# Kernel tuning notes

Hardware: AMD Instinct MI355X
Metric: run time of the kernel (lower is better)

## Reference

```python
import jax, jax.numpy as jnp
import numpy as np
from itertools import chain, combinations

OBS_DIM = 4096
LAT = 64
NG = 4
GS = OBS_DIM // NG  # 1024 features per group (round-robin i % NG == g)
B = 8192


def _powerset_mask(n):
    subsets = list(chain.from_iterable(combinations(range(n), r) for r in range(1, n + 1)))
    m = np.zeros((len(subsets), n), np.float32)
    for i, s in enumerate(subsets):
        m[i, list(s)] = 1.0
    return jnp.asarray(m)


SUBSET_MASK = _powerset_mask(NG)  # [S, G], S = 2^G - 1 = 15
GROUP_IDX = jnp.asarray(np.stack([np.arange(g, OBS_DIM, NG) for g in range(NG)]), dtype=jnp.int32)  # [G, GS]


def setup_inputs() -> dict:
    key = jax.random.key(0)
    ks = jax.random.split(key, 11)
    s = 0.05
    H = 2 * LAT  # encoder hidden / output width
    return {
        "X": jax.random.normal(ks[0], (B, OBS_DIM), jnp.float32),
        "eps": jax.random.normal(ks[1], (B, LAT), jnp.float32),
        "subset_idx": jax.random.randint(ks[2], (B,), 0, SUBSET_MASK.shape[0], dtype=jnp.int32),
        "enc_w1": jax.random.normal(ks[3], (NG, GS, H), jnp.float32) * s,
        "enc_b1": jnp.zeros((NG, H), jnp.float32),
        "enc_w2": jax.random.normal(ks[4], (NG, H, H), jnp.float32) * s,
        "enc_b2": jnp.zeros((NG, H), jnp.float32),
        "dec_w1": jax.random.normal(ks[5], (NG, LAT, LAT), jnp.float32) * s,
        "dec_b1": jnp.zeros((NG, LAT), jnp.float32),
        "dec_w2": jax.random.normal(ks[6], (NG, LAT, GS), jnp.float32) * s,
        "dec_b2": jnp.zeros((NG, GS), jnp.float32),
    }


def reference(X, eps, subset_idx, enc_w1, enc_b1, enc_w2, enc_b2, dec_w1, dec_b1, dec_w2, dec_b2):
    # ---- encode: per-group gather + tiny MLP (depth=2) ----
    Xg = X[:, GROUP_IDX]  # [B, G, GS] gather of group columns
    h = jax.nn.relu(jnp.einsum('bgi,gih->bgh', Xg, enc_w1) + enc_b1[None])  # [B, G, 2L]
    ml = jnp.einsum('bgh,gho->bgo', h, enc_w2) + enc_b2[None]               # [B, G, 2L]
    means, logvars = jnp.split(ml, 2, axis=-1)  # each [B, G, L]
    means = jnp.transpose(means, (0, 2, 1))     # [B, L, G] (tf stacks groups on axis=2)
    logvars = jnp.transpose(logvars, (0, 2, 1))

    # ---- mopoe: PoE over every non-empty subset of groups ----
    taus = jnp.exp(-logvars)                                   # [B, L, G]
    tau = jnp.einsum('blg,sg->bls', taus, SUBSET_MASK) + 1.0   # [B, L, S] (normalize_outp=True adds 1)
    m_means = jnp.einsum('blg,sg->bls', taus * means, SUBSET_MASK) / tau
    m_logvars = -jnp.log(tau)                                  # log(1/tau)

    # ---- reparameterize: pick one random subset per batch row ----
    sel = subset_idx[:, None, None].astype(jnp.int32)          # [B, 1, 1]
    smean = jnp.take_along_axis(m_means, sel, axis=-1)[..., 0]    # [B, L]
    slogv = jnp.take_along_axis(m_logvars, sel, axis=-1)[..., 0]  # [B, L]
    z = smean + eps * jnp.exp(0.5 * slogv)                     # [B, L]

    # ---- decode: per-group tiny MLP, scatter back to obs_dim ----
    hd = jax.nn.relu(jnp.einsum('bl,glm->bgm', z, dec_w1) + dec_b1[None])  # [B, G, L]
    outg = jnp.einsum('bgm,gmo->bgo', hd, dec_w2) + dec_b2[None]            # [B, G, GS]
    recon = jnp.zeros((X.shape[0], OBS_DIM), X.dtype).at[:, GROUP_IDX.reshape(-1)].set(
        outg.reshape(X.shape[0], -1))
    return recon
```

## Files before the change

### kernel.cpp

```cpp
#include <hip/hip_runtime.h>
#include <hip/hip_bf16.h>
#include <math.h>

#define B_TOT 8192
#define OBS   4096
#define NG    4
#define GSZ   1024
#define LATD  64
#define HDIM  128

typedef __attribute__((ext_vector_type(8))) short   short8_t;
typedef __attribute__((ext_vector_type(8))) unsigned short ushort8_t;
typedef __attribute__((ext_vector_type(4))) float   float4_t;

__constant__ int kMask[15] = {1,2,4,8, 3,5,9,6,10,12, 7,11,13,14, 15};

static __device__ __forceinline__ unsigned short f2b(float x) {
  __hip_bfloat16 b = __float2bfloat16(x);
  return *reinterpret_cast<unsigned short*>(&b);
}
static __device__ __forceinline__ unsigned int pack2(float lo, float hi) {
  return (unsigned int)f2b(lo) | ((unsigned int)f2b(hi) << 16);
}

#define N1 524288
#define N2 65536
#define N4 262144
__global__ __launch_bounds__(256) void k_prep(const float* __restrict__ w1,
                                              const float* __restrict__ w2,
                                              const float* __restrict__ w4,
                                              unsigned short* __restrict__ W1t,
                                              unsigned short* __restrict__ W2t,
                                              unsigned short* __restrict__ W4t) {
  const int i = blockIdx.x * 256 + threadIdx.x;
  if (i < N1) {
    const int g = i >> 17, rem = i & 131071;
    const int h = rem >> 10, k = rem & 1023;
    W1t[i] = f2b(w1[g * 131072 + k * 128 + h]);
  } else if (i < N1 + N2) {
    const int idx = i - N1;
    const int g = idx >> 14, rem = idx & 16383;
    const int o = rem >> 7, k = rem & 127;
    W2t[idx] = f2b(w2[g * 16384 + k * 128 + o]);
  } else {
    const int idx = i - N1 - N2;
    const int g = idx >> 16, rem = idx & 65535;
    const int o = rem >> 6, k = rem & 63;
    W4t[idx] = f2b(w4[g * 65536 + k * 1024 + o]);
  }
}

__global__ __launch_bounds__(512, 2) void k_enc1(const float* __restrict__ X,
                                                 const unsigned short* __restrict__ W1t,
                                                 const float* __restrict__ B1,
                                                 unsigned short* __restrict__ Hbf) {
  __shared__ unsigned short lA[4][4][32][40];

  const int tid = threadIdx.x;
  const int w   = tid >> 6;
  const int l   = tid & 63;
  const int g   = w >> 1;
  const int hh  = (w & 1) * 64;
  const int r0b = blockIdx.x * 32;
  const int l15 = l & 15;
  const int oct = l >> 4;

  const int sr  = tid >> 4;
  const int skk = tid & 15;

  const float* xrow = X + (size_t)(r0b + sr) * OBS;

  float4 q[4][2];
#pragma unroll
  for (int sub = 0; sub < 4; ++sub) {
    const float* p = xrow + sub * 128 + skk * 8;
    q[sub][0] = *(const float4*)(p);
    q[sub][1] = *(const float4*)(p + 4);
  }

  float4_t acc[2][4];
#pragma unroll
  for (int i = 0; i < 2; ++i)
#pragma unroll
    for (int j = 0; j < 4; ++j) acc[i][j] = (float4_t){0.f, 0.f, 0.f, 0.f};

  for (int c = 0; c < 8; ++c) {
#pragma unroll
    for (int sub = 0; sub < 4; ++sub) {
      const float a0[4] = {q[sub][0].x, q[sub][0].y, q[sub][0].z, q[sub][0].w};
      const float a1[4] = {q[sub][1].x, q[sub][1].y, q[sub][1].z, q[sub][1].w};
#pragma unroll
      for (int gg = 0; gg < 4; ++gg)
        *(unsigned int*)(&lA[sub][gg][sr][skk * 2]) = pack2(a0[gg], a1[gg]);
    }
    __syncthreads();

    if (c < 7) {
      const float* base = xrow + (c + 1) * 512;
#pragma unroll
      for (int sub = 0; sub < 4; ++sub) {
        const float* p = base + sub * 128 + skk * 8;
        q[sub][0] = *(const float4*)(p);
        q[sub][1] = *(const float4*)(p + 4);
      }
    }

#pragma unroll
    for (int sub = 0; sub < 4; ++sub) {
      short8_t af[2], bf[4];
#pragma unroll
      for (int mi = 0; mi < 2; ++mi)
        af[mi] = *(const short8_t*)((const char*)&lA[sub][g][0][0] +
                                    (mi * 16 + l15) * 80 + oct * 16);
#pragma unroll
      for (int ni = 0; ni < 4; ++ni)
        bf[ni] = *(const short8_t*)(W1t +
                  (size_t)(g * 128 + hh + ni * 16 + l15) * 1024 +
                  c * 128 + sub * 32 + oct * 8);
#pragma unroll
      for (int mi = 0; mi < 2; ++mi)
#pragma unroll
        for (int ni = 0; ni < 4; ++ni)
          acc[mi][ni] = __builtin_amdgcn_mfma_f32_16x16x32_bf16(af[mi], bf[ni], acc[mi][ni], 0, 0, 0);
    }
    __syncthreads();
  }

#pragma unroll
  for (int ni = 0; ni < 4; ++ni) {
    const int col = g * 128 + hh + ni * 16 + l15;
    const float b = B1[col];
#pragma unroll
    for (int mi = 0; mi < 2; ++mi) {
      const int rbase = r0b + mi * 16 + oct * 4;
#pragma unroll
      for (int j = 0; j < 4; ++j)
        Hbf[(size_t)(rbase + j) * 512 + col] = f2b(fmaxf(acc[mi][ni][j] + b, 0.0f));
    }
  }
}

struct Enc2Lds {
  union {
    unsigned short A[16][1288];
    float mls[32][516];
  };
};
__global__ __launch_bounds__(512, 2) void k_enc2_samp(const unsigned short* __restrict__ Hbf,
                                                      const unsigned short* __restrict__ W2t,
                                                      const float* __restrict__ B2,
                                                      const float* __restrict__ eps,
                                                      const int*   __restrict__ subset_idx,
                                                      float* __restrict__ Z) {
  __shared__ Enc2Lds u;
  const int tid = threadIdx.x;
  const int w   = tid >> 6;
  const int l   = tid & 63;
  const int g   = w >> 1;
  const int hh  = (w & 1) * 64;
  const int rb  = blockIdx.x * 32;
  const int l15 = l & 15;
  const int oct = l >> 4;

#pragma unroll
  for (int i = 0; i < 4; ++i) {
    const int q   = tid + i * 512;
    const int row = q >> 6;
    const int co  = (q & 63) * 8;
    const int gg  = co >> 7;
    const int cg  = co & 127;
    const int ks  = cg >> 5;
    const int off = cg & 31;
    const ushort8_t v = *(const ushort8_t*)(Hbf + (size_t)(rb + row) * 512 + co);
    *(ushort8_t*)(&u.A[ks * 4 + gg][row * 40 + off]) = v;
  }
  __syncthreads();

  float4_t acc[2][4];
#pragma unroll
  for (int i = 0; i < 2; ++i)
#pragma unroll
    for (int j = 0; j < 4; ++j) acc[i][j] = (float4_t){0.f, 0.f, 0.f, 0.f};

#pragma unroll
  for (int ks = 0; ks < 4; ++ks) {
    short8_t af[2], bf[4];
#pragma unroll
    for (int mi = 0; mi < 2; ++mi)
      af[mi] = *(const short8_t*)(&u.A[ks * 4 + g][(mi * 16 + l15) * 40 + oct * 8]);
#pragma unroll
    for (int ni = 0; ni < 4; ++ni)
      bf[ni] = *(const short8_t*)(W2t +
                (size_t)(g * 128 + hh + ni * 16 + l15) * 128 + ks * 32 + oct * 8);
#pragma unroll
    for (int mi = 0; mi < 2; ++mi)
#pragma unroll
      for (int ni = 0; ni < 4; ++ni)
        acc[mi][ni] = __builtin_amdgcn_mfma_f32_16x16x32_bf16(af[mi], bf[ni], acc[mi][ni], 0, 0, 0);
  }
  __syncthreads();

#pragma unroll
  for (int ni = 0; ni < 4; ++ni) {
    const int col = g * 128 + hh + ni * 16 + l15;
    const float b = B2[col];
#pragma unroll
    for (int mi = 0; mi < 2; ++mi)
#pragma unroll
      for (int j = 0; j < 4; ++j)
        u.mls[mi * 16 + oct * 4 + j][col] = acc[mi][ni][j] + b;
  }
  __syncthreads();

#pragma unroll
  for (int q = 0; q < 4; ++q) {
    const int idx = q * 512 + tid;
    const int r   = idx >> 6;
    const int ll  = idx & 63;
    const int m   = kMask[subset_idx[rb + r]];
    float tau = 1.0f, num = 0.0f;
#pragma unroll
    for (int gg = 0; gg < 4; ++gg) {
      if (m & (1 << gg)) {
        const float lv = u.mls[r][gg * 128 + 64 + ll];
        const float mu = u.mls[r][gg * 128 + ll];
        const float t  = expf(-lv);
        tau += t;
        num = fmaf(t, mu, num);
      }
    }
    Z[(size_t)(rb + r) * LATD + ll] =
        num / tau + eps[(size_t)(rb + r) * LATD + ll] * rsqrtf(tau);
  }
}

__global__ __launch_bounds__(256) void k_dec1(const float* __restrict__ Z,
                                              const float* __restrict__ W,
                                              const float* __restrict__ Bb,
                                              unsigned short* __restrict__ Hd) {
  const int tid  = threadIdx.x;
  const int wid  = tid >> 6;
  const int lane = tid & 63;
  const int r0   = blockIdx.x * 16 + wid * 4;
  const int c0   = lane * 4;
  const int g    = c0 >> 6;
  const int m0   = c0 & 63;

  const float* Wp = W + (size_t)g * LATD * LATD + m0;
  const float* Ap = Z + (size_t)r0 * LATD;

  float acc[4][4];
#pragma unroll
  for (int i = 0; i < 4; ++i)
#pragma unroll
    for (int j = 0; j < 4; ++j) acc[i][j] = 0.0f;

#pragma unroll 4
  for (int k = 0; k < LATD; ++k) {
    const float4 wv = *(const float4*)(Wp + (size_t)k * LATD);
    float a[4];
#pragma unroll
    for (int i = 0; i < 4; ++i) a[i] = Ap[(size_t)i * LATD + k];
#pragma unroll
    for (int i = 0; i < 4; ++i) {
      acc[i][0] = fmaf(a[i], wv.x, acc[i][0]);
      acc[i][1] = fmaf(a[i], wv.y, acc[i][1]);
      acc[i][2] = fmaf(a[i], wv.z, acc[i][2]);
      acc[i][3] = fmaf(a[i], wv.w, acc[i][3]);
    }
  }

  const float4 ba = *(const float4*)(Bb + c0);
#pragma unroll
  for (int i = 0; i < 4; ++i) {
    ushort4 o;
    o.x = f2b(fmaxf(acc[i][0] + ba.x, 0.0f));
    o.y = f2b(fmaxf(acc[i][1] + ba.y, 0.0f));
    o.z = f2b(fmaxf(acc[i][2] + ba.z, 0.0f));
    o.w = f2b(fmaxf(acc[i][3] + ba.w, 0.0f));
    *(ushort4*)(Hd + (size_t)(r0 + i) * 256 + c0) = o;
  }
}

__global__ __launch_bounds__(512) void k_dec2(const unsigned short* __restrict__ Hd,
                                              const unsigned short* __restrict__ W4t,
                                              const float* __restrict__ Bb,
                                              float* __restrict__ Out) {
  __shared__ float obuf[32][264];

  const int tid = threadIdx.x;
  const int w   = tid >> 6;
  const int l   = tid & 63;
  const int g   = w >> 1;
  const int ohh = (w & 1) * 32;
  const int r0  = blockIdx.x * 32;
  const int ob  = blockIdx.y * 64;
  const int l15 = l & 15;
  const int oct = l >> 4;

  float4_t acc[2][2];
#pragma unroll
  for (int i = 0; i < 2; ++i)
#pragma unroll
    for (int j = 0; j < 2; ++j) acc[i][j] = (float4_t){0.f, 0.f, 0.f, 0.f};

#pragma unroll
  for (int ks = 0; ks < 2; ++ks) {
    short8_t af[2], bf[2];
#pragma unroll
    for (int mi = 0; mi < 2; ++mi)
      af[mi] = *(const short8_t*)(Hd + (size_t)(r0 + mi * 16 + l15) * 256 +
                                  g * 64 + ks * 32 + oct * 8);
#pragma unroll
    for (int ni = 0; ni < 2; ++ni)
      bf[ni] = *(const short8_t*)(W4t + (size_t)(g * 1024 + ob + ohh + ni * 16 + l15) * 64 +
                                  ks * 32 + oct * 8);
#pragma unroll
    for (int mi = 0; mi < 2; ++mi)
#pragma unroll
      for (int ni = 0; ni < 2; ++ni)
        acc[mi][ni] = __builtin_amdgcn_mfma_f32_16x16x32_bf16(af[mi], bf[ni], acc[mi][ni], 0, 0, 0);
  }

#pragma unroll
  for (int ni = 0; ni < 2; ++ni) {
    const int lo = ohh + ni * 16 + l15;
    const float b = Bb[g * 1024 + ob + lo];
#pragma unroll
    for (int mi = 0; mi < 2; ++mi) {
      const int rloc = mi * 16 + oct * 4;
#pragma unroll
      for (int j = 0; j < 4; ++j)
        obuf[rloc + j][4 * lo + g] = acc[mi][ni][j] + b;
    }
  }
  __syncthreads();

#pragma unroll
  for (int i = 0; i < 4; ++i) {
    const int q = tid + i * 512;
    const int row = q >> 6, c4 = q & 63;
    const float4 v = *(const float4*)&obuf[row][c4 * 4];
    *(float4*)(Out + (size_t)(r0 + row) * OBS + 4 * ob + c4 * 4) = v;
  }
}

extern "C" void kernel_launch(void* const* d_in, const int* in_sizes, int n_in,
                              void* d_out, int out_size, void* d_ws, size_t ws_size,
                              hipStream_t stream) {
  const float* X          = (const float*)d_in[0];
  const float* eps        = (const float*)d_in[1];
  const int*   subset_idx = (const int*)  d_in[2];
  const float* enc_w1     = (const float*)d_in[3];
  const float* enc_b1     = (const float*)d_in[4];
  const float* enc_w2     = (const float*)d_in[5];
  const float* enc_b2     = (const float*)d_in[6];
  const float* dec_w1     = (const float*)d_in[7];
  const float* dec_b1     = (const float*)d_in[8];
  const float* dec_w2     = (const float*)d_in[9];
  const float* dec_b2     = (const float*)d_in[10];
  float* out = (float*)d_out;

  char* wsb = (char*)d_ws;
  unsigned short* Hbf = (unsigned short*)wsb;
  float*          z   = (float*)(wsb + (8u  << 20));
  unsigned short* Hd  = (unsigned short*)(wsb + (10u << 20));
  unsigned short* W1t = (unsigned short*)(wsb + (14u << 20));
  unsigned short* W2t = (unsigned short*)(wsb + (15u << 20));
  unsigned short* W4t = (unsigned short*)(wsb + (15u << 20) + (512u << 10));

  k_prep<<<3328, 256, 0, stream>>>(enc_w1, enc_w2, dec_w2, W1t, W2t, W4t);
  k_enc1<<<256, 512, 0, stream>>>(X, W1t, enc_b1, Hbf);
  k_enc2_samp<<<256, 512, 0, stream>>>(Hbf, W2t, enc_b2, eps, subset_idx, z);
  k_dec1<<<512, 256, 0, stream>>>(z, dec_w1, dec_b1, Hd);
  k_dec2<<<dim3(256, 16), 512, 0, stream>>>(Hd, W4t, dec_b2, out);
}
```

Measured before the change: 127.3 us.

## Fuse encoder layers, sampling and first decoder layer; pre-convert X to bf16

Adds a separate pass that converts X to bf16 in a group-deinterleaved layout written to workspace. The two encoder GEMMs, the PoE sampling and the first decoder layer are merged into one kernel. The first decoder layer now runs on MFMA using a prepared bf16 weight instead of scalar fp32 FMAs. This removes the Hbf and z round-trips and two launches. In exchange it writes and re-reads a 64MB bf16 copy of X, and the first-layer GEMM loses its LDS staging and register prefetch, so it now reads strided rows straight from global memory.

```diff
diff --git a/kernel.cpp b/kernel.cpp
--- a/kernel.cpp
+++ b/kernel.cpp
@@ -25,12 +25,15 @@
 
 #define N1 524288
 #define N2 65536
+#define N3 16384
 #define N4 262144
 __global__ __launch_bounds__(256) void k_prep(const float* __restrict__ w1,
                                               const float* __restrict__ w2,
+                                              const float* __restrict__ w3,
                                               const float* __restrict__ w4,
                                               unsigned short* __restrict__ W1t,
                                               unsigned short* __restrict__ W2t,
+                                              unsigned short* __restrict__ W3t,
                                               unsigned short* __restrict__ W4t) {
   const int i = blockIdx.x * 256 + threadIdx.x;
   if (i < N1) {
@@ -42,117 +45,52 @@
     const int g = idx >> 14, rem = idx & 16383;
     const int o = rem >> 7, k = rem & 127;
     W2t[idx] = f2b(w2[g * 16384 + k * 128 + o]);
-  } else {
+  } else if (i < N1 + N2 + N3) {
     const int idx = i - N1 - N2;
+    const int g = idx >> 12, rem = idx & 4095;
+    const int m = rem >> 6, k = rem & 63;
+    W3t[idx] = f2b(w3[g * 4096 + k * 64 + m]);
+  } else if (i < N1 + N2 + N3 + N4) {
+    const int idx = i - N1 - N2 - N3;
     const int g = idx >> 16, rem = idx & 65535;
     const int o = rem >> 6, k = rem & 63;
     W4t[idx] = f2b(w4[g * 65536 + k * 1024 + o]);
   }
 }
 
-__global__ __launch_bounds__(512, 2) void k_enc1(const float* __restrict__ X,
-                                                 const unsigned short* __restrict__ W1t,
-                                                 const float* __restrict__ B1,
-                                                 unsigned short* __restrict__ Hbf) {
-  __shared__ unsigned short lA[4][4][32][40];
-
-  const int tid = threadIdx.x;
-  const int w   = tid >> 6;
-  const int l   = tid & 63;
-  const int g   = w >> 1;
-  const int hh  = (w & 1) * 64;
-  const int r0b = blockIdx.x * 32;
-  const int l15 = l & 15;
-  const int oct = l >> 4;
-
-  const int sr  = tid >> 4;
-  const int skk = tid & 15;
-
-  const float* xrow = X + (size_t)(r0b + sr) * OBS;
-
-  float4 q[4][2];
-#pragma unroll
-  for (int sub = 0; sub < 4; ++sub) {
-    const float* p = xrow + sub * 128 + skk * 8;
-    q[sub][0] = *(const float4*)(p);
-    q[sub][1] = *(const float4*)(p + 4);
-  }
-
-  float4_t acc[2][4];
-#pragma unroll
-  for (int i = 0; i < 2; ++i)
-#pragma unroll
-    for (int j = 0; j < 4; ++j) acc[i][j] = (float4_t){0.f, 0.f, 0.f, 0.f};
-
-  for (int c = 0; c < 8; ++c) {
-#pragma unroll
-    for (int sub = 0; sub < 4; ++sub) {
-      const float a0[4] = {q[sub][0].x, q[sub][0].y, q[sub][0].z, q[sub][0].w};
-      const float a1[4] = {q[sub][1].x, q[sub][1].y, q[sub][1].z, q[sub][1].w};
-#pragma unroll
-      for (int gg = 0; gg < 4; ++gg)
-        *(unsigned int*)(&lA[sub][gg][sr][skk * 2]) = pack2(a0[gg], a1[gg]);
-    }
-    __syncthreads();
-
-    if (c < 7) {
-      const float* base = xrow + (c + 1) * 512;
-#pragma unroll
-      for (int sub = 0; sub < 4; ++sub) {
-        const float* p = base + sub * 128 + skk * 8;
-        q[sub][0] = *(const float4*)(p);
-        q[sub][1] = *(const float4*)(p + 4);
-      }
-    }
-
-#pragma unroll
-    for (int sub = 0; sub < 4; ++sub) {
-      short8_t af[2], bf[4];
-#pragma unroll
-      for (int mi = 0; mi < 2; ++mi)
-        af[mi] = *(const short8_t*)((const char*)&lA[sub][g][0][0] +
-                                    (mi * 16 + l15) * 80 + oct * 16);
-#pragma unroll
-      for (int ni = 0; ni < 4; ++ni)
-        bf[ni] = *(const short8_t*)(W1t +
-                  (size_t)(g * 128 + hh + ni * 16 + l15) * 1024 +
-                  c * 128 + sub * 32 + oct * 8);
-#pragma unroll
-      for (int mi = 0; mi < 2; ++mi)
-#pragma unroll
-        for (int ni = 0; ni < 4; ++ni)
-          acc[mi][ni] = __builtin_amdgcn_mfma_f32_16x16x32_bf16(af[mi], bf[ni], acc[mi][ni], 0, 0, 0);
-    }
-    __syncthreads();
-  }
-
-#pragma unroll
-  for (int ni = 0; ni < 4; ++ni) {
-    const int col = g * 128 + hh + ni * 16 + l15;
-    const float b = B1[col];
-#pragma unroll
-    for (int mi = 0; mi < 2; ++mi) {
-      const int rbase = r0b + mi * 16 + oct * 4;
-#pragma unroll
-      for (int j = 0; j < 4; ++j)
-        Hbf[(size_t)(rbase + j) * 512 + col] = f2b(fmaxf(acc[mi][ni][j] + b, 0.0f));
-    }
-  }
-}
-
-struct Enc2Lds {
+__global__ __launch_bounds__(512) void k_prepx(const float* __restrict__ X,
+                                               unsigned short* __restrict__ Xt) {
+  const int b = blockIdx.x;
+  const int t = threadIdx.x;
+  const float* p = X + (size_t)b * OBS + t * 8;
+  const float4 f0 = *(const float4*)(p);
+  const float4 f1 = *(const float4*)(p + 4);
+  const float a0[4] = {f0.x, f0.y, f0.z, f0.w};
+  const float a1[4] = {f1.x, f1.y, f1.z, f1.w};
+  unsigned int* q = (unsigned int*)(Xt + (size_t)b * OBS);
+#pragma unroll
+  for (int g = 0; g < 4; ++g)
+    q[g * 512 + t] = pack2(a0[g], a1[g]);
+}
+
+struct EncLds {
   union {
-    unsigned short A[16][1288];
+    unsigned short hp[16][32][40];
     float mls[32][516];
-  };
+  } u;
+  unsigned short zb[32][72];
 };
-__global__ __launch_bounds__(512, 2) void k_enc2_samp(const unsigned short* __restrict__ Hbf,
-                                                      const unsigned short* __restrict__ W2t,
-                                                      const float* __restrict__ B2,
-                                                      const float* __restrict__ eps,
-                                                      const int*   __restrict__ subset_idx,
-                                                      float* __restrict__ Z) {
-  __shared__ Enc2Lds u;
+__global__ __launch_bounds__(512, 2) void k_enc(const unsigned short* __restrict__ Xt,
+                                                const unsigned short* __restrict__ W1t,
+                                                const unsigned short* __restrict__ W2t,
+                                                const unsigned short* __restrict__ W3t,
+                                                const float* __restrict__ B1,
+                                                const float* __restrict__ B2,
+                                                const float* __restrict__ DB1,
+                                                const float* __restrict__ eps,
+                                                const int*   __restrict__ subset_idx,
+                                                unsigned short* __restrict__ Hd) {
+  __shared__ EncLds s;
   const int tid = threadIdx.x;
   const int w   = tid >> 6;
   const int l   = tid & 63;
@@ -162,41 +100,69 @@
   const int l15 = l & 15;
   const int oct = l >> 4;
 
-#pragma unroll
-  for (int i = 0; i < 4; ++i) {
-    const int q   = tid + i * 512;
-    const int row = q >> 6;
-    const int co  = (q & 63) * 8;
-    const int gg  = co >> 7;
-    const int cg  = co & 127;
-    const int ks  = cg >> 5;
-    const int off = cg & 31;
-    const ushort8_t v = *(const ushort8_t*)(Hbf + (size_t)(rb + row) * 512 + co);
-    *(ushort8_t*)(&u.A[ks * 4 + gg][row * 40 + off]) = v;
-  }
-  __syncthreads();
-
   float4_t acc[2][4];
 #pragma unroll
   for (int i = 0; i < 2; ++i)
 #pragma unroll
     for (int j = 0; j < 4; ++j) acc[i][j] = (float4_t){0.f, 0.f, 0.f, 0.f};
 
-#pragma unroll
-  for (int ks = 0; ks < 4; ++ks) {
-    short8_t af[2], bf[4];
-#pragma unroll
-    for (int mi = 0; mi < 2; ++mi)
-      af[mi] = *(const short8_t*)(&u.A[ks * 4 + g][(mi * 16 + l15) * 40 + oct * 8]);
-#pragma unroll
-    for (int ni = 0; ni < 4; ++ni)
-      bf[ni] = *(const short8_t*)(W2t +
-                (size_t)(g * 128 + hh + ni * 16 + l15) * 128 + ks * 32 + oct * 8);
-#pragma unroll
-    for (int mi = 0; mi < 2; ++mi)
+  {
+    const unsigned short* abase = Xt + (size_t)(rb + l15) * OBS + g * GSZ + oct * 8;
+    const unsigned short* bbase = W1t + (size_t)(g * 128 + hh + l15) * GSZ + oct * 8;
+#pragma unroll 4
+    for (int ks = 0; ks < 32; ++ks) {
+      short8_t af[2], bf[4];
+#pragma unroll
+      for (int mi = 0; mi < 2; ++mi)
+        af[mi] = *(const short8_t*)(abase + (size_t)mi * 16 * OBS + ks * 32);
 #pragma unroll
       for (int ni = 0; ni < 4; ++ni)
-        acc[mi][ni] = __builtin_amdgcn_mfma_f32_16x16x32_bf16(af[mi], bf[ni], acc[mi][ni], 0, 0, 0);
+        bf[ni] = *(const short8_t*)(bbase + (size_t)ni * 16 * GSZ + ks * 32);
+#pragma unroll
+      for (int mi = 0; mi < 2; ++mi)
+#pragma unroll
+        for (int ni = 0; ni < 4; ++ni)
+          acc[mi][ni] = __builtin_amdgcn_mfma_f32_16x16x32_bf16(af[mi], bf[ni], acc[mi][ni], 0, 0, 0);
+    }
+  }
+
+#pragma unroll
+  for (int ni = 0; ni < 4; ++ni) {
+    const int cg    = hh + ni * 16 + l15;
+    const int plane = (cg >> 5) * 4 + g;
+    const int off   = cg & 31;
+    const float b   = B1[g * 128 + cg];
+#pragma unroll
+    for (int mi = 0; mi < 2; ++mi) {
+      const int row = mi * 16 + oct * 4;
+#pragma unroll
+      for (int j = 0; j < 4; ++j)
+        s.u.hp[plane][row + j][off] = f2b(fmaxf(acc[mi][ni][j] + b, 0.0f));
+    }
+  }
+  __syncthreads();
+
+#pragma unroll
+  for (int i = 0; i < 2; ++i)
+#pragma unroll
+    for (int j = 0; j < 4; ++j) acc[i][j] = (float4_t){0.f, 0.f, 0.f, 0.f};
+  {
+    const unsigned short* bbase = W2t + (size_t)(g * 128 + hh + l15) * HDIM + oct * 8;
+#pragma unroll
+    for (int ks = 0; ks < 4; ++ks) {
+      short8_t af[2], bf[4];
+#pragma unroll
+      for (int mi = 0; mi < 2; ++mi)
+        af[mi] = *(const short8_t*)(&s.u.hp[ks * 4 + g][mi * 16 + l15][oct * 8]);
+#pragma unroll
+      for (int ni = 0; ni < 4; ++ni)
+        bf[ni] = *(const short8_t*)(bbase + (size_t)ni * 16 * HDIM + ks * 32);
+#pragma unroll
+      for (int mi = 0; mi < 2; ++mi)
+#pragma unroll
+        for (int ni = 0; ni < 4; ++ni)
+          acc[mi][ni] = __builtin_amdgcn_mfma_f32_16x16x32_bf16(af[mi], bf[ni], acc[mi][ni], 0, 0, 0);
+    }
   }
   __syncthreads();
 
@@ -208,7 +174,7 @@
     for (int mi = 0; mi < 2; ++mi)
 #pragma unroll
       for (int j = 0; j < 4; ++j)
-        u.mls[mi * 16 + oct * 4 + j][col] = acc[mi][ni][j] + b;
+        s.u.mls[mi * 16 + oct * 4 + j][col] = acc[mi][ni][j] + b;
   }
   __syncthreads();
 
@@ -222,63 +188,53 @@
 #pragma unroll
     for (int gg = 0; gg < 4; ++gg) {
       if (m & (1 << gg)) {
-        const float lv = u.mls[r][gg * 128 + 64 + ll];
-        const float mu = u.mls[r][gg * 128 + ll];
+        const float lv = s.u.mls[r][gg * 128 + 64 + ll];
+        const float mu = s.u.mls[r][gg * 128 + ll];
         const float t  = expf(-lv);
         tau += t;
         num = fmaf(t, mu, num);
       }
     }
-    Z[(size_t)(rb + r) * LATD + ll] =
-        num / tau + eps[(size_t)(rb + r) * LATD + ll] * rsqrtf(tau);
-  }
-}
-
-__global__ __launch_bounds__(256) void k_dec1(const float* __restrict__ Z,
-                                              const float* __restrict__ W,
-                                              const float* __restrict__ Bb,
-                                              unsigned short* __restrict__ Hd) {
-  const int tid  = threadIdx.x;
-  const int wid  = tid >> 6;
-  const int lane = tid & 63;
-  const int r0   = blockIdx.x * 16 + wid * 4;
-  const int c0   = lane * 4;
-  const int g    = c0 >> 6;
-  const int m0   = c0 & 63;
-
-  const float* Wp = W + (size_t)g * LATD * LATD + m0;
-  const float* Ap = Z + (size_t)r0 * LATD;
-
-  float acc[4][4];
-#pragma unroll
-  for (int i = 0; i < 4; ++i)
-#pragma unroll
-    for (int j = 0; j < 4; ++j) acc[i][j] = 0.0f;
-
-#pragma unroll 4
-  for (int k = 0; k < LATD; ++k) {
-    const float4 wv = *(const float4*)(Wp + (size_t)k * LATD);
-    float a[4];
-#pragma unroll
-    for (int i = 0; i < 4; ++i) a[i] = Ap[(size_t)i * LATD + k];
-#pragma unroll
-    for (int i = 0; i < 4; ++i) {
-      acc[i][0] = fmaf(a[i], wv.x, acc[i][0]);
-      acc[i][1] = fmaf(a[i], wv.y, acc[i][1]);
-      acc[i][2] = fmaf(a[i], wv.z, acc[i][2]);
-      acc[i][3] = fmaf(a[i], wv.w, acc[i][3]);
-    }
-  }
-
-  const float4 ba = *(const float4*)(Bb + c0);
-#pragma unroll
-  for (int i = 0; i < 4; ++i) {
-    ushort4 o;
-    o.x = f2b(fmaxf(acc[i][0] + ba.x, 0.0f));
-    o.y = f2b(fmaxf(acc[i][1] + ba.y, 0.0f));
-    o.z = f2b(fmaxf(acc[i][2] + ba.z, 0.0f));
-    o.w = f2b(fmaxf(acc[i][3] + ba.w, 0.0f));
-    *(ushort4*)(Hd + (size_t)(r0 + i) * 256 + c0) = o;
+    const float zv = num / tau + eps[(size_t)(rb + r) * LATD + ll] * rsqrtf(tau);
+    s.zb[r][ll] = f2b(zv);
+  }
+  __syncthreads();
+
+  const int mh = (w & 1) * 32;
+  float4_t a3[2][2];
+#pragma unroll
+  for (int i = 0; i < 2; ++i)
+#pragma unroll
+    for (int j = 0; j < 2; ++j) a3[i][j] = (float4_t){0.f, 0.f, 0.f, 0.f};
+  {
+    const unsigned short* bbase = W3t + (size_t)(g * 64 + mh + l15) * LATD + oct * 8;
+#pragma unroll
+    for (int ks = 0; ks < 2; ++ks) {
+      short8_t af[2], bf[2];
+#pragma unroll
+      for (int mi = 0; mi < 2; ++mi)
+        af[mi] = *(const short8_t*)(&s.zb[mi * 16 + l15][ks * 32 + oct * 8]);
+#pragma unroll
+      for (int ni = 0; ni < 2; ++ni)
+        bf[ni] = *(const short8_t*)(bbase + (size_t)ni * 16 * LATD + ks * 32);
+#pragma unroll
+      for (int mi = 0; mi < 2; ++mi)
+#pragma unroll
+        for (int ni = 0; ni < 2; ++ni)
+          a3[mi][ni] = __builtin_amdgcn_mfma_f32_16x16x32_bf16(af[mi], bf[ni], a3[mi][ni], 0, 0, 0);
+    }
+  }
+#pragma unroll
+  for (int ni = 0; ni < 2; ++ni) {
+    const int col = g * 64 + mh + ni * 16 + l15;
+    const float b = DB1[col];
+#pragma unroll
+    for (int mi = 0; mi < 2; ++mi) {
+      const int row = mi * 16 + oct * 4;
+#pragma unroll
+      for (int j = 0; j < 4; ++j)
+        Hd[(size_t)(rb + row + j) * 256 + col] = f2b(fmaxf(a3[mi][ni][j] + b, 0.0f));
+    }
   }
 }
 
@@ -362,16 +318,17 @@
   float* out = (float*)d_out;
 
   char* wsb = (char*)d_ws;
-  unsigned short* Hbf = (unsigned short*)wsb;
-  float*          z   = (float*)(wsb + (8u  << 20));
-  unsigned short* Hd  = (unsigned short*)(wsb + (10u << 20));
-  unsigned short* W1t = (unsigned short*)(wsb + (14u << 20));
-  unsigned short* W2t = (unsigned short*)(wsb + (15u << 20));
-  unsigned short* W4t = (unsigned short*)(wsb + (15u << 20) + (512u << 10));
-
-  k_prep<<<3328, 256, 0, stream>>>(enc_w1, enc_w2, dec_w2, W1t, W2t, W4t);
-  k_enc1<<<256, 512, 0, stream>>>(X, W1t, enc_b1, Hbf);
-  k_enc2_samp<<<256, 512, 0, stream>>>(Hbf, W2t, enc_b2, eps, subset_idx, z);
-  k_dec1<<<512, 256, 0, stream>>>(z, dec_w1, dec_b1, Hd);
+  unsigned short* Xt  = (unsigned short*)wsb;
+  unsigned short* Hd  = (unsigned short*)(wsb + (64u << 20));
+  unsigned short* W1t = (unsigned short*)(wsb + (68u << 20));
+  unsigned short* W2t = (unsigned short*)(wsb + (69u << 20));
+  unsigned short* W3t = (unsigned short*)(wsb + (69u << 20) + (128u << 10));
+  unsigned short* W4t = (unsigned short*)(wsb + (69u << 20) + (160u << 10));
+
+  k_prep<<<3392, 256, 0, stream>>>(enc_w1, enc_w2, dec_w1, dec_w2,
+                                   W1t, W2t, W3t, W4t);
+  k_prepx<<<8192, 512, 0, stream>>>(X, Xt);
+  k_enc<<<256, 512, 0, stream>>>(Xt, W1t, W2t, W3t, enc_b1, enc_b2, dec_b1,
+                                 eps, subset_idx, Hd);
   k_dec2<<<dim3(256, 16), 512, 0, stream>>>(Hd, W4t, dec_b2, out);
 }
```

Measured after the change: 149.6 us. +17.5%, slower.
